# Kernel optimization log

Hardware: AMD Instinct MI355X
Metric: run time of the kernel (lower is better)

The kernel has to match this reference:

```python
import jax, jax.numpy as jnp
import numpy as np
from jax import lax

REGION_SIZE = 5      # local window side (init kwarg)
BANDWIDTH = 0.1      # KDE kernel bandwidth (init kwarg)
NUM_BINS = 256       # intensity histogram bins
EPS = 1e-10


def setup_inputs() -> dict:
    key = jax.random.key(0)
    # image-like inputs in [0, 255] to match the 256 intensity bins
    x = jax.random.uniform(key, (8, 3, 96, 96), dtype=jnp.float32) * 255.0
    return {"x": x}


def reference(x):
    # x: [B, C, H, W]
    bins = jnp.arange(NUM_BINS, dtype=x.dtype)            # [256]
    # derivative-of-sigmoid KDE kernel evaluated at each (pixel, bin) pair
    d = (x[..., None] - bins) / BANDWIDTH                 # [B,C,H,W,256]
    sig = jax.nn.sigmoid(d)
    k = sig * (1.0 - sig)                                 # [B,C,H,W,256]
    # accumulate kernel mass over the region_size x region_size window
    # (stride 1, centered -> SAME padding), per bin
    p = lax.reduce_window(
        k, jnp.float32(0.0), lax.add,
        window_dimensions=(1, 1, REGION_SIZE, REGION_SIZE, 1),
        window_strides=(1, 1, 1, 1, 1),
        padding='SAME')                                   # [B,C,H,W,256]
    # normalize to a probability distribution over bins
    p = p / (jnp.sum(p, axis=-1, keepdims=True) + EPS)
    # Shannon entropy per pixel
    return -jnp.sum(p * jnp.log(p + EPS), axis=-1)        # [B,C,H,W]
```

## Files before the change

kernel.cpp:

```cpp
#include <hip/hip_runtime.h>
#include <stdint.h>


#define W 96
#define H 96
#define TPB 256

__global__ __launch_bounds__(TPB) void entropy_kde_kernel(
    const float* __restrict__ x, float* __restrict__ out, int total)
{
    const int pid = blockIdx.x * TPB + threadIdx.x;
    if (pid >= total) return;

    const int xcol = pid % W;
    const int y    = (pid / W) % H;
    const int img  = pid / (W * H);
    const float* __restrict__ base = x + img * (H * W);

    int   b0a[25];
    float k0a[25], k1a[25];
    float S = 0.f, T = 0.f;

    #pragma unroll
    for (int i = 0; i < 25; ++i) {
        const int dy = i / 5 - 2, dx = i % 5 - 2;
        const int yy = y + dy,    xx = xcol + dx;
        const bool ok = (yy >= 0) & (yy < H) & (xx >= 0) & (xx < W);
        const float v = base[min(max(yy, 0), H - 1) * W + min(max(xx, 0), W - 1)];

        const int   b0 = (int)v;
        const float f  = v - (float)b0;
        const float E  = __expf(-10.f * f);
        const float E2 = __expf(10.f * f - 10.f);
        const float r0 = __builtin_amdgcn_rcpf(1.f + E);
        const float r1 = __builtin_amdgcn_rcpf(1.f + E2);
        const float k0 = ok ? E  * r0 * r0 : 0.f;
        const float k1 = ok ? E2 * r1 * r1 : 0.f;

        float P0 = 0.f, P1 = 0.f;
        #pragma unroll
        for (int j = 0; j < i; ++j) {
            const int d = b0 - b0a[j];
            P0 += (d == 0) ? k0a[j] : ((d ==  1) ? k1a[j] : 0.f);
            P1 += (d == 0) ? k1a[j] : ((d == -1) ? k0a[j] : 0.f);
        }

        const float z0 = P0 + k0, z1 = P1 + k1;
        T += z0 * __logf(z0 + 1e-10f) - P0 * __logf(P0 + 1e-10f)
           + z1 * __logf(z1 + 1e-10f) - P1 * __logf(P1 + 1e-10f);
        S += k0 + k1;

        b0a[i] = b0; k0a[i] = k0; k1a[i] = k1;
    }

    const float Sp = S + 1e-10f;
    out[pid] = __logf(Sp) - T / Sp;
}

extern "C" void kernel_launch(void* const* d_in, const int* in_sizes, int n_in,
                              void* d_out, int out_size, void* d_ws, size_t ws_size,
                              hipStream_t stream)
{
    const float* x = (const float*)d_in[0];
    float* out = (float*)d_out;
    const int total  = in_sizes[0];
    const int blocks = (total + TPB - 1) / TPB;
    entropy_kde_kernel<<<blocks, TPB, 0, stream>>>(x, out, total);
}
```

Baseline: 82.04 us.

## Pack kernel masses into half2 and accumulate pairwise bin sums in fp16

Loads all 25 window values up front, then packs the two per-neighbor kernel masses into a half2 register. The pairwise bin-match accumulation uses packed fp16 adds with shift-based selection, which halves the register footprint and the number of add instructions in the O(25^2) inner loop. The entropy sum is split across four independent accumulators to shorten the dependency chain. This trades precision for speed: fp16 rounding of the kernel masses and of the partial sums may change the output accuracy.

```diff
diff --git a/kernel.cpp b/kernel.cpp
--- a/kernel.cpp
+++ b/kernel.cpp
@@ -1,4 +1,5 @@
 #include <hip/hip_runtime.h>
+#include <hip/hip_fp16.h>
 #include <stdint.h>
 
 
@@ -17,17 +18,23 @@
     const int img  = pid / (W * H);
     const float* __restrict__ base = x + img * (H * W);
 
-    int   b0a[25];
-    float k0a[25], k1a[25];
-    float S = 0.f, T = 0.f;
+    float va[25];
+    #pragma unroll
+    for (int i = 0; i < 25; ++i) {
+        const int dy = i / 5 - 2, dx = i % 5 - 2;
+        const int yy = y + dy,    xx = xcol + dx;
+        va[i] = base[min(max(yy, 0), H - 1) * W + min(max(xx, 0), W - 1)];
+    }
 
+    int      b0a[25];
+    uint32_t pk [25];
+    float S = 0.f;
     #pragma unroll
     for (int i = 0; i < 25; ++i) {
         const int dy = i / 5 - 2, dx = i % 5 - 2;
         const int yy = y + dy,    xx = xcol + dx;
         const bool ok = (yy >= 0) & (yy < H) & (xx >= 0) & (xx < W);
-        const float v = base[min(max(yy, 0), H - 1) * W + min(max(xx, 0), W - 1)];
-
+        const float v  = va[i];
         const int   b0 = (int)v;
         const float f  = v - (float)b0;
         const float E  = __expf(-10.f * f);
@@ -36,23 +43,40 @@
         const float r1 = __builtin_amdgcn_rcpf(1.f + E2);
         const float k0 = ok ? E  * r0 * r0 : 0.f;
         const float k1 = ok ? E2 * r1 * r1 : 0.f;
+        const __half2 hk = __floats2half2_rn(k0, k1);
+        const float2  kc = __half22float2(hk);
+        S += kc.x + kc.y;
+        b0a[i] = b0;
+        pk[i]  = __builtin_bit_cast(uint32_t, hk);
+    }
 
-        float P0 = 0.f, P1 = 0.f;
+    float T0 = 0.f, T1 = 0.f, T2 = 0.f, T3 = 0.f;
+    #pragma unroll
+    for (int i = 0; i < 25; ++i) {
+        const int b0i = b0a[i];
+        uint32_t Ppk = 0u;
         #pragma unroll
         for (int j = 0; j < i; ++j) {
-            const int d = b0 - b0a[j];
-            P0 += (d == 0) ? k0a[j] : ((d ==  1) ? k1a[j] : 0.f);
-            P1 += (d == 0) ? k1a[j] : ((d == -1) ? k0a[j] : 0.f);
+            const int d = b0i - b0a[j];
+            const uint32_t pj = pk[j];
+            uint32_t t = (d == 0)  ? pj         : 0u;
+            t          = (d == 1)  ? (pj >> 16) : t;
+            t          = (d == -1) ? (pj << 16) : t;
+            const __half2 sum = __hadd2(__builtin_bit_cast(__half2, Ppk),
+                                        __builtin_bit_cast(__half2, t));
+            Ppk = __builtin_bit_cast(uint32_t, sum);
         }
-
-        const float z0 = P0 + k0, z1 = P1 + k1;
-        T += z0 * __logf(z0 + 1e-10f) - P0 * __logf(P0 + 1e-10f)
-           + z1 * __logf(z1 + 1e-10f) - P1 * __logf(P1 + 1e-10f);
-        S += k0 + k1;
-
-        b0a[i] = b0; k0a[i] = k0; k1a[i] = k1;
+        const float2 P  = __half22float2(__builtin_bit_cast(__half2, Ppk));
+        const float2 kc = __half22float2(__builtin_bit_cast(__half2, pk[i]));
+        const float z0 = P.x + kc.x, z1 = P.y + kc.y;
+        const float t4 = z0  * __logf(z0  + 1e-10f) - P.x * __logf(P.x + 1e-10f)
+                       + z1  * __logf(z1  + 1e-10f) - P.y * __logf(P.y + 1e-10f);
+        if      ((i & 3) == 0) T0 += t4;
+        else if ((i & 3) == 1) T1 += t4;
+        else if ((i & 3) == 2) T2 += t4;
+        else                   T3 += t4;
     }
-
+    const float T  = (T0 + T1) + (T2 + T3);
     const float Sp = S + 1e-10f;
     out[pid] = __logf(Sp) - T / Sp;
 }
```

Result: slower. 85.56 us (+4.3%).

## Precompute padded per-pixel kernel mass and use packed half2 shift-select accumulation

Applied to the files above, without the earlier changes.

Splits the work into two kernels. The first computes each pixel's two nonzero bin masses once into a zero-padded workspace, so the stencil no longer needs boundary checks. The second kernel replaces the compare/select neighbour matching with a 64-bit shift of packed half2 masses, accumulates with half2 adds, and uses log2 with split accumulators. This removes the 25x redundant exp/rcp work per output and cuts VALU ops in the O(n^2) loop, at the cost of an extra launch, a workspace round trip, and reduced precision from fp16 masses in the partial sums.

```diff
diff --git a/kernel.cpp b/kernel.cpp
--- a/kernel.cpp
+++ b/kernel.cpp
@@ -1,60 +1,100 @@
 #include <hip/hip_runtime.h>
+#include <hip/hip_fp16.h>
 #include <stdint.h>
 
 
-#define W 96
-#define H 96
+#define W   96
+#define H   96
+#define WP  100
+#define IMG (W*H)
+#define IMGP (WP*WP)
 #define TPB 256
 
-__global__ __launch_bounds__(TPB) void entropy_kde_kernel(
-    const float* __restrict__ x, float* __restrict__ out, int total)
+__global__ __launch_bounds__(TPB) void mass_kernel(
+    const float* __restrict__ x, uint4* __restrict__ wm, int total2)
 {
     const int pid = blockIdx.x * TPB + threadIdx.x;
-    if (pid >= total) return;
+    if (pid >= total2) return;
+    const int x2  = pid % WP;
+    const int y2  = (pid / WP) % WP;
+    const int img = pid / IMGP;
 
-    const int xcol = pid % W;
-    const int y    = (pid / W) % H;
-    const int img  = pid / (W * H);
-    const float* __restrict__ base = x + img * (H * W);
-
-    int   b0a[25];
-    float k0a[25], k1a[25];
-    float S = 0.f, T = 0.f;
-
-    #pragma unroll
-    for (int i = 0; i < 25; ++i) {
-        const int dy = i / 5 - 2, dx = i % 5 - 2;
-        const int yy = y + dy,    xx = xcol + dx;
-        const bool ok = (yy >= 0) & (yy < H) & (xx >= 0) & (xx < W);
-        const float v = base[min(max(yy, 0), H - 1) * W + min(max(xx, 0), W - 1)];
-
+    uint4 e;
+    if (x2 >= 2 && x2 < WP - 2 && y2 >= 2 && y2 < WP - 2) {
+        const float v  = x[img * IMG + (y2 - 2) * W + (x2 - 2)];
         const int   b0 = (int)v;
         const float f  = v - (float)b0;
         const float E  = __expf(-10.f * f);
         const float E2 = __expf(10.f * f - 10.f);
         const float r0 = __builtin_amdgcn_rcpf(1.f + E);
         const float r1 = __builtin_amdgcn_rcpf(1.f + E2);
-        const float k0 = ok ? E  * r0 * r0 : 0.f;
-        const float k1 = ok ? E2 * r1 * r1 : 0.f;
+        const float k0 = E  * r0 * r0;
+        const float k1 = E2 * r1 * r1;
+        const __half2 hk = __floats2half2_rn(k0, k1);
+        const float2  kc = __half22float2(hk);
+        e.x = __builtin_bit_cast(uint32_t, hk);
+        e.y = (uint32_t)b0;
+        e.z = __builtin_bit_cast(uint32_t, kc.x);
+        e.w = __builtin_bit_cast(uint32_t, kc.y);
+    } else {
+        e.x = 0u;
+        e.y = (uint32_t)(int)(-32768);
+        e.z = 0u;
+        e.w = 0u;
+    }
+    wm[pid] = e;
+}
 
-        float P0 = 0.f, P1 = 0.f;
+__global__ __launch_bounds__(TPB) void entropy_kde_kernel(
+    const uint4* __restrict__ wm, float* __restrict__ out)
+{
+    const int px   = blockIdx.x * TPB + threadIdx.x;
+    const int xcol = px % W;
+    const int y    = (px / W) % H;
+    const int img  = px / IMG;
+    const uint4* __restrict__ wb = wm + img * IMGP + y * WP + xcol;
+
+    uint64_t pk64[25];
+    int      b0a [25];
+    float S0 = 0.f, S1 = 0.f;
+    float T0 = 0.f, T1 = 0.f, T2a = 0.f, T3 = 0.f;
+
+    #pragma unroll
+    for (int i = 0; i < 25; ++i) {
+        const int dy = i / 5, dx = i % 5;
+        const uint4 m = wb[dy * WP + dx];
+        const int   b0i = (int)m.y;
+        const float k0  = __builtin_bit_cast(float, m.z);
+        const float k1  = __builtin_bit_cast(float, m.w);
+        if (i & 1) S1 += k0 + k1; else S0 += k0 + k1;
+
+        uint32_t Ppk = 0u;
         #pragma unroll
         for (int j = 0; j < i; ++j) {
-            const int d = b0 - b0a[j];
-            P0 += (d == 0) ? k0a[j] : ((d ==  1) ? k1a[j] : 0.f);
-            P1 += (d == 0) ? k1a[j] : ((d == -1) ? k0a[j] : 0.f);
+            const int d = b0i - b0a[j];
+            int s = (d << 4) + 32;
+            s = s < 0 ? 0 : (s > 63 ? 63 : s);
+            const uint32_t t = (uint32_t)(pk64[j] >> s);
+            const __half2 sum = __hadd2(__builtin_bit_cast(__half2, Ppk),
+                                        __builtin_bit_cast(__half2, t));
+            Ppk = __builtin_bit_cast(uint32_t, sum);
         }
+        const float2 P  = __half22float2(__builtin_bit_cast(__half2, Ppk));
+        const float z0 = P.x + k0, z1 = P.y + k1;
+        const float t4 = z0  * __log2f(z0  + 1e-10f) - P.x * __log2f(P.x + 1e-10f)
+                       + z1  * __log2f(z1  + 1e-10f) - P.y * __log2f(P.y + 1e-10f);
+        if      ((i & 3) == 0) T0  += t4;
+        else if ((i & 3) == 1) T1  += t4;
+        else if ((i & 3) == 2) T2a += t4;
+        else                   T3  += t4;
 
-        const float z0 = P0 + k0, z1 = P1 + k1;
-        T += z0 * __logf(z0 + 1e-10f) - P0 * __logf(P0 + 1e-10f)
-           + z1 * __logf(z1 + 1e-10f) - P1 * __logf(P1 + 1e-10f);
-        S += k0 + k1;
-
-        b0a[i] = b0; k0a[i] = k0; k1a[i] = k1;
+        b0a[i]  = b0i;
+        pk64[i] = ((uint64_t)m.x) << 32;
     }
 
-    const float Sp = S + 1e-10f;
-    out[pid] = __logf(Sp) - T / Sp;
+    const float S  = (S0 + S1) + 1e-10f;
+    const float T  = (T0 + T1) + (T2a + T3);
+    out[px] = 0.69314718056f * (__log2f(S) - T / S);
 }
 
 extern "C" void kernel_launch(void* const* d_in, const int* in_sizes, int n_in,
@@ -63,7 +103,9 @@
 {
     const float* x = (const float*)d_in[0];
     float* out = (float*)d_out;
+    uint4* wm  = (uint4*)d_ws;
     const int total  = in_sizes[0];
-    const int blocks = (total + TPB - 1) / TPB;
-    entropy_kde_kernel<<<blocks, TPB, 0, stream>>>(x, out, total);
+    const int total2 = (total / IMG) * IMGP;
+    mass_kernel<<<(total2 + TPB - 1) / TPB, TPB, 0, stream>>>(x, wm, total2);
+    entropy_kde_kernel<<<total / TPB, TPB, 0, stream>>>(wm, out);
 }
```

New measurement: 73.45 us. -10.5%, faster.
